# Performance work log

Hardware: AMD Instinct MI355X
Metric: run time of the kernel (lower is better)

## Reference

```python
import jax, jax.numpy as jnp
import numpy as np
import math

D_MODEL = 1024
FEAT = 16            # feature_dim
HEADS = 16
HEAD_DIM = D_MODEL // HEADS          # 64
EXP = 1 + FEAT + FEAT * FEAT         # 273, expanded (Taylor) feature dim
BATCH = 4
SEQ = 2048


def taylor_exp(x):
    """2nd-order Taylor feature map: [1, x/d^{1/4}, (x ox x)/(sqrt(2)*sqrt(d))]."""
    d = x.shape[-1]
    r2 = math.sqrt(2.0)
    rd = math.sqrt(d)
    rrd = math.sqrt(rd)
    x2 = (x[..., :, None] * x[..., None, :]).reshape(*x.shape[:-1], d * d) / r2
    return jnp.concatenate([jnp.ones_like(x[..., :1]), x / rrd, x2 / rd], axis=-1)


def setup_inputs() -> dict:
    key = jax.random.key(0)
    ks = jax.random.split(key, 9)
    s_in = 1.0 / math.sqrt(D_MODEL)
    inp = {
        "x": jax.random.normal(ks[0], (BATCH, SEQ, D_MODEL), dtype=jnp.float32),
        "kv_state": jnp.zeros((BATCH, HEADS, EXP, HEAD_DIM), dtype=jnp.float32),
        "k_state": jnp.zeros((BATCH, HEADS, EXP), dtype=jnp.float32),
        # Linear params stored as [in, out] (y = x @ W + b)
        "Wq": jax.random.normal(ks[1], (D_MODEL, FEAT * HEADS), dtype=jnp.float32) * s_in,
        "bq": jnp.zeros((FEAT * HEADS,), dtype=jnp.float32),
        "Wk": jax.random.normal(ks[2], (D_MODEL, FEAT * HEADS), dtype=jnp.float32) * s_in,
        "bk": jnp.zeros((FEAT * HEADS,), dtype=jnp.float32),
        "Wv": jax.random.normal(ks[3], (D_MODEL, HEAD_DIM * HEADS), dtype=jnp.float32) * s_in,
        "bv": jnp.zeros((HEAD_DIM * HEADS,), dtype=jnp.float32),
        "Wo": jax.random.normal(ks[4], (HEADS * HEAD_DIM, D_MODEL), dtype=jnp.float32) * s_in,
        "bo": jnp.zeros((D_MODEL,), dtype=jnp.float32),
    }
    return inp


def _forward(x, kv_state, k_state, Wq, bq, Wk, bk, Wv, bv, Wo, bo):
    b, l, _ = x.shape
    # projections -> b h l d
    q = (x @ Wq + bq).reshape(b, l, HEADS, FEAT).transpose(0, 2, 1, 3)
    k = (x @ Wk + bk).reshape(b, l, HEADS, FEAT).transpose(0, 2, 1, 3)
    v = (x @ Wv + bv).reshape(b, l, HEADS, HEAD_DIM).transpose(0, 2, 1, 3)
    q = taylor_exp(q)  # b h l EXP
    k = taylor_exp(k)  # b h l EXP

    # scan over time: carry (kv_state [b,h,EXP,hd], k_state [b,h,EXP])
    qs = jnp.moveaxis(q, 2, 0)  # l b h EXP
    ks = jnp.moveaxis(k, 2, 0)  # l b h EXP
    vs = jnp.moveaxis(v, 2, 0)  # l b h hd

    def step(carry, qkv_t):
        kv, kst = carry
        q_t, k_t, v_t = qkv_t
        kv = kv + k_t[..., :, None] * v_t[..., None, :]   # b h EXP hd
        kst = kst + k_t                                    # b h EXP
        num = jnp.einsum('bhd,bhdc->bhc', q_t, kv)
        den = jnp.einsum('bhd,bhd->bh', q_t, kst) + 1e-6
        return (kv, kst), num / den[..., None]

    (kv_f, kst_f), outs = jax.lax.scan(step, (kv_state, k_state), (qs, ks, vs))
    # outs: l b h hd -> b l (h hd)
    y = jnp.moveaxis(outs, 0, 1).reshape(b, l, HEADS * HEAD_DIM)
    y = y @ Wo + bo  # dropout is identity in eval mode
    return y, kv_f, kst_f


def reference(x, kv_state, k_state, Wq, bq, Wk, bk, Wv, bv, Wo, bo):
    return _forward(x, kv_state, k_state, Wq, bq, Wk, bk, Wv, bv, Wo, bo)
```

## Files before the change

### kernel.cpp

```cpp
#include <hip/hip_runtime.h>

typedef unsigned short u16;
typedef __attribute__((ext_vector_type(8))) short bf16x8;
typedef __attribute__((ext_vector_type(4))) float f32x4;

#define BATCH 4
#define SEQ   2048
#define DM    1024
#define HEADS 16
#define FEAT  16
#define HD    64
#define EXPD  273
#define EXPP  288
#define CHK   128
#define NC    16
#define BH    64
#define QKS   512
#define MROWS 8192
#define C2    0.17677669529663687f

__device__ __forceinline__ u16 f2b(float f) {
  union { float f; unsigned u; } v; v.f = f;
  unsigned u = v.u;
  return (u16)((u + 0x7fffu + ((u >> 16) & 1u)) >> 16);
}
__device__ __forceinline__ float b2f(u16 s) {
  union { unsigned u; float f; } v; v.u = ((unsigned)s) << 16; return v.f;
}

typedef const unsigned int __attribute__((address_space(1)))* gas1;
typedef unsigned int __attribute__((address_space(3)))* las3;
__device__ __forceinline__ void gl_lds16(const u16* g, u16* l) {
  __builtin_amdgcn_global_load_lds((gas1)(const void*)g, (las3)(void*)l, 16, 0, 0);
}

__global__ __launch_bounds__(256) void prep(const float* __restrict__ x, u16* __restrict__ xb,
                                            const float* __restrict__ Wq, const float* __restrict__ Wk,
                                            const float* __restrict__ Wv, const float* __restrict__ Wo,
                                            u16* __restrict__ wqkT, u16* __restrict__ wvT, u16* __restrict__ woT,
                                            const float* __restrict__ bq, const float* __restrict__ bk,
                                            float* __restrict__ bqk) {
  __shared__ float tile[32][33];
  int id = blockIdx.x;
  if (id < 8192) {
    int i = id * 256 + threadIdx.x;
    float4 v = ((const float4*)x)[i];
    u16 r[4] = {f2b(v.x), f2b(v.y), f2b(v.z), f2b(v.w)};
    ((uint2*)xb)[i] = *(uint2*)r;
    return;
  }
  id -= 8192;
  if (id < 2560) {
    const float* src; u16* dst; int N, t;
    if (id < 256)       { src = Wq; dst = wqkT;            N = 256;  t = id; }
    else if (id < 512)  { src = Wk; dst = wqkT + 256 * DM; N = 256;  t = id - 256; }
    else if (id < 1536) { src = Wv; dst = wvT;             N = 1024; t = id - 512; }
    else                { src = Wo; dst = woT;             N = 1024; t = id - 1536; }
    int nt = N / 32;
    int n0 = (t % nt) * 32, k0 = (t / nt) * 32;
    int tx = threadIdx.x & 31, ty = threadIdx.x >> 5;
    for (int i = ty; i < 32; i += 8)
      tile[i][tx] = src[(size_t)(k0 + i) * N + n0 + tx];
    __syncthreads();
    for (int i = ty; i < 32; i += 8)
      dst[(size_t)(n0 + i) * DM + k0 + tx] = f2b(tile[tx][i]);
    return;
  }
  int i = threadIdx.x;
  bqk[i] = bq[i];
  bqk[256 + i] = bk[i];
}

__global__ __launch_bounds__(256) void gemm128(const u16* __restrict__ A, const u16* __restrict__ BT,
                                               const float* __restrict__ bias, int M, int N, int K,
                                               float* __restrict__ outF, u16* __restrict__ outB,
                                               u16* __restrict__ outT) {
  __shared__ __align__(16) u16 As[128 * 32];
  __shared__ __align__(16) u16 Bs[128 * 32];
  const int tid = threadIdx.x;
  const int wave = tid >> 6, lane = tid & 63, qd = lane >> 4, ln = lane & 15;
  const int wr = (wave >> 1) * 64, wc = (wave & 1) * 64;
  const int m0 = blockIdx.y * 128, n0 = blockIdx.x * 128;
  f32x4 acc[4][4];
#pragma unroll
  for (int i = 0; i < 4; i++)
#pragma unroll
    for (int j = 0; j < 4; j++) acc[i][j] = (f32x4){0.f, 0.f, 0.f, 0.f};
  const int sr = tid >> 2, sk = (tid & 3) * 8;
  const u16* gA0 = A + (size_t)(m0 + sr) * K + sk;
  const u16* gA1 = A + (size_t)(m0 + 64 + sr) * K + sk;
  const u16* gB0 = BT + (size_t)(n0 + sr) * K + sk;
  const u16* gB1 = BT + (size_t)(n0 + 64 + sr) * K + sk;
  u16* lA0 = &As[(size_t)(wave * 64) * 8];
  u16* lA1 = &As[(size_t)(256 + wave * 64) * 8];
  u16* lB0 = &Bs[(size_t)(wave * 64) * 8];
  u16* lB1 = &Bs[(size_t)(256 + wave * 64) * 8];
  for (int kk = 0; kk < K; kk += 32) {
    gl_lds16(gA0 + kk, lA0);
    gl_lds16(gA1 + kk, lA1);
    gl_lds16(gB0 + kk, lB0);
    gl_lds16(gB1 + kk, lB1);
    __syncthreads();
    bf16x8 af[4], bf[4];
#pragma unroll
    for (int t = 0; t < 4; t++) {
      af[t] = *(const bf16x8*)&As[(wr + t * 16 + ln) * 32 + qd * 8];
      bf[t] = *(const bf16x8*)&Bs[(wc + t * 16 + ln) * 32 + qd * 8];
    }
#pragma unroll
    for (int mt = 0; mt < 4; mt++)
#pragma unroll
      for (int nt = 0; nt < 4; nt++)
        acc[mt][nt] = __builtin_amdgcn_mfma_f32_16x16x32_bf16(af[mt], bf[nt], acc[mt][nt], 0, 0, 0);
    __syncthreads();
  }
  if (outT) {
#pragma unroll
    for (int nt = 0; nt < 4; nt++) {
      int col = n0 + wc + nt * 16 + ln;
      float bv = bias[col];
#pragma unroll
      for (int mt = 0; mt < 4; mt++) {
        u16 pk[4];
#pragma unroll
        for (int r = 0; r < 4; r++) pk[r] = f2b(acc[mt][nt][r] + bv);
        int row0 = m0 + wr + mt * 16 + qd * 4;
        *(uint2*)&outT[(size_t)col * M + row0] = *(uint2*)pk;
      }
    }
    return;
  }
#pragma unroll
  for (int nt = 0; nt < 4; nt++) {
    int col = n0 + wc + nt * 16 + ln;
    float bv = bias[col];
#pragma unroll
    for (int mt = 0; mt < 4; mt++) {
#pragma unroll
      for (int r = 0; r < 4; r++) {
        int row = m0 + wr + mt * 16 + qd * 4 + r;
        float v = acc[mt][nt][r] + bv;
        if (outF) outF[(size_t)row * N + col] = v;
        else      outB[(size_t)row * N + col] = f2b(v);
      }
    }
  }
}

template<int KT>
__device__ __forceinline__ void feat_row(const float* q16, int p, u16* dst) {
  u16 pk[16];
  if (KT == 0 && p == 0) {
    pk[0] = 0x3F80;
#pragma unroll
    for (int j = 1; j < 16; j++) pk[j] = f2b(0.5f * q16[j - 1]);
  } else if (KT == 0) {
    pk[0] = f2b(0.5f * q16[15]);
    float wm = C2 * q16[0];
#pragma unroll
    for (int j = 1; j < 16; j++) pk[j] = f2b(wm * q16[j - 1]);
  } else {
    constexpr int c = 2 * KT;
    float wm = C2 * (p ? q16[c]     : q16[c - 1]);
    float w0 = C2 * (p ? q16[c - 1] : q16[c - 2]);
    pk[0] = f2b(w0 * q16[15]);
#pragma unroll
    for (int j = 1; j < 16; j++) pk[j] = f2b(wm * q16[j - 1]);
    if (KT == 8 && p) {
#pragma unroll
      for (int j = 1; j < 16; j++) pk[j] = 0;
    }
  }
  *(uint4*)dst = *(uint4*)pk;
  *(uint4*)(dst + 8) = *(uint4*)(pk + 8);
}

template<int MTB>
__device__ __forceinline__ void kfeat(const float* k16, int p, int t2, u16 (*kfT)[16][136]) {
  u16 pk[16];
  if (MTB == 0 && true) {
    if (p == 0) {
      pk[0] = 0x3F80;
#pragma unroll
      for (int j = 1; j < 16; j++) pk[j] = f2b(0.5f * k16[j - 1]);
    } else {
      float w0 = C2 * k16[0], wm = C2 * k16[1];
      pk[0] = f2b(w0 * k16[15]);
#pragma unroll
      for (int j = 1; j < 16; j++) pk[j] = f2b(wm * k16[j - 1]);
    }
  } else if (MTB == 1) {
    if (p == 0) {
      pk[0] = f2b(0.5f * k16[15]);
      float wm = C2 * k16[0];
#pragma unroll
      for (int j = 1; j < 16; j++) pk[j] = f2b(wm * k16[j - 1]);
    } else {
      float w0 = C2 * k16[1], wm = C2 * k16[2];
      pk[0] = f2b(w0 * k16[15]);
#pragma unroll
      for (int j = 1; j < 16; j++) pk[j] = f2b(wm * k16[j - 1]);
    }
  } else {
    float wm = C2 * (p ? k16[MTB + 1] : k16[MTB - 1]);
    float w0 = C2 * (p ? k16[MTB]     : k16[MTB - 2]);
    pk[0] = f2b(w0 * k16[15]);
#pragma unroll
    for (int j = 1; j < 16; j++) pk[j] = f2b(wm * k16[j - 1]);
  }
  int b = 2 * p + (MTB & 1);
#pragma unroll
  for (int el = 0; el < 16; el++) kfT[b][el][t2] = pk[el];
}

__global__ __launch_bounds__(256) void chunk_sums(const float* __restrict__ qkw, const u16* __restrict__ vbT,
                                                  u16* __restrict__ ckvT, float* __restrict__ ck) {
  __shared__ float kl[CHK][20];
  __shared__ __align__(16) u16 kfT[4][16][136];
  const int tid = threadIdx.x;
  const int bh = blockIdx.x / NC, c = blockIdx.x % NC;
  const int b = bh >> 4, h = bh & 15;
  const int wave = tid >> 6, lane = tid & 63, qd = lane >> 4, ln = lane & 15;
  const int t2 = tid >> 1, p = tid & 1;
  const size_t rowbase = (size_t)(b * SEQ + c * CHK);
  float k16[16];
  {
    const float* kp = &qkw[(rowbase + t2) * QKS + 256 + h * FEAT];
    float4 v0 = *(const float4*)kp, v1 = *(const float4*)(kp + 4);
    float4 v2 = *(const float4*)(kp + 8), v3 = *(const float4*)(kp + 12);
    k16[0] = v0.x; k16[1] = v0.y; k16[2] = v0.z; k16[3] = v0.w;
    k16[4] = v1.x; k16[5] = v1.y; k16[6] = v1.z; k16[7] = v1.w;
    k16[8] = v2.x; k16[9] = v2.y; k16[10] = v2.z; k16[11] = v2.w;
    k16[12] = v3.x; k16[13] = v3.y; k16[14] = v3.z; k16[15] = v3.w;
    float4 h0, h1;
    if (p == 0) { h0 = v0; h1 = v1; } else { h0 = v2; h1 = v3; }
    *(float4*)&kl[t2][p * 8] = h0;
    *(float4*)&kl[t2][p * 8 + 4] = h1;
  }
  uint4 bVv[4][4];
#pragma unroll
  for (int kk2 = 0; kk2 < 4; kk2++)
#pragma unroll
    for (int nt = 0; nt < 4; nt++)
      bVv[kk2][nt] = *(const uint4*)&vbT[(size_t)(h * HD + nt * 16 + ln) * MROWS +
                                         rowbase + kk2 * 32 + qd * 8];
  const size_t obase = (size_t)(bh * NC + c) * HD;
  auto mstore = [&](int mt, int bufw) {
    f32x4 acc[4];
#pragma unroll
    for (int nt = 0; nt < 4; nt++) acc[nt] = (f32x4){0.f, 0.f, 0.f, 0.f};
#pragma unroll
    for (int kk2 = 0; kk2 < 4; kk2++) {
      bf16x8 a = *(const bf16x8*)&kfT[bufw][ln][kk2 * 32 + qd * 8];
#pragma unroll
      for (int nt = 0; nt < 4; nt++) {
        bf16x8 bb = *(const bf16x8*)&bVv[kk2][nt];
        acc[nt] = __builtin_amdgcn_mfma_f32_16x16x32_bf16(a, bb, acc[nt], 0, 0, 0);
      }
    }
#pragma unroll
    for (int nt = 0; nt < 4; nt++) {
      u16 pk[4];
#pragma unroll
      for (int r = 0; r < 4; r++) pk[r] = f2b(acc[nt][r]);
      *(uint2*)&ckvT[(obase + nt * 16 + ln) * EXPP + mt * 16 + qd * 4] = *(uint2*)pk;
    }
  };
  __syncthreads();
  kfeat<0>(k16, p, t2, kfT); kfeat<1>(k16, p, t2, kfT);
  __syncthreads();
  mstore(wave, wave);
  __syncthreads();
  kfeat<4>(k16, p, t2, kfT); kfeat<5>(k16, p, t2, kfT);
  __syncthreads();
  mstore(4 + wave, wave);
  __syncthreads();
  kfeat<8>(k16, p, t2, kfT); kfeat<9>(k16, p, t2, kfT);
  __syncthreads();
  mstore(8 + wave, wave);
  __syncthreads();
  kfeat<12>(k16, p, t2, kfT); kfeat<13>(k16, p, t2, kfT);
  __syncthreads();
  mstore(12 + wave, wave);
  __syncthreads();
  {
    u16 pk[16];
    if (p == 0) {
      float w0 = C2 * k16[14], wm = C2 * k16[15];
      pk[0] = f2b(w0 * k16[15]);
#pragma unroll
      for (int j = 1; j < 16; j++) pk[j] = f2b(wm * k16[j - 1]);
    } else {
      pk[0] = f2b(C2 * k16[15] * k16[15]);
#pragma unroll
      for (int j = 1; j < 16; j++) pk[j] = 0;
    }
#pragma unroll
    for (int el = 0; el < 16; el++) kfT[p][el][t2] = pk[el];
  }
  __syncthreads();
  if (wave < 2) mstore(16 + wave, wave);
  for (int e = tid; e < EXPP; e += 256) {
    float s = 0.f;
    if (e == 0) s = (float)CHK;
    else if (e < 17) { float t = 0.f; for (int tt = 0; tt < CHK; tt++) t += kl[tt][e - 1]; s = 0.5f * t; }
    else if (e < EXPD) {
      int u = e - 17, i0 = u >> 4, j0 = u & 15; float t = 0.f;
      for (int tt = 0; tt < CHK; tt++) t += kl[tt][i0] * kl[tt][j0];
      s = C2 * t;
    }
    ck[(size_t)(bh * NC + c) * EXPP + e] = s;
  }
}

__global__ __launch_bounds__(256) void kv_prefix(u16* __restrict__ ckvT, const float* __restrict__ kv0,
                                                 float* __restrict__ out_kv,
                                                 float* __restrict__ ck, const float* __restrict__ k0,
                                                 float* __restrict__ out_k) {
  const int tid = threadIdx.x;
  const int bh = blockIdx.x / 10, eg = blockIdx.x % 10;
  if (eg == 9) {
    for (int e = tid; e < EXPP; e += 256) {
      float S = (e < EXPD) ? k0[(size_t)bh * EXPD + e] : 0.f;
      for (int c = 0; c < NC; c++) {
        size_t idx = ((size_t)bh * NC + c) * EXPP + e;
        float v = ck[idx];
        ck[idx] = S;
        S += v;
      }
      if (e < EXPD) out_k[(size_t)bh * EXPD + e] = S;
    }
    return;
  }
  const int hd = tid >> 2;
  const int e0 = eg * 32 + (tid & 3) * 8;
  float S[8];
#pragma unroll
  for (int j = 0; j < 8; j++) {
    int e = e0 + j;
    S[j] = (e < EXPD) ? kv0[((size_t)bh * EXPD + e) * HD + hd] : 0.f;
  }
  u16* base = ckvT + ((size_t)bh * NC * HD + hd) * EXPP + e0;
  const size_t cstride = (size_t)HD * EXPP;
  uint4 v0 = *(const uint4*)base;
  uint4 v1 = *(const uint4*)(base + cstride);
  for (int c = 0; c < NC; c++) {
    uint4 vn = v1;
    if (c + 2 < NC) vn = *(const uint4*)(base + (size_t)(c + 2) * cstride);
    union { uint4 q; u16 s[8]; } pk;
#pragma unroll
    for (int j = 0; j < 8; j++) pk.s[j] = f2b(S[j]);
    *(uint4*)(base + (size_t)c * cstride) = pk.q;
    union { uint4 q; u16 s[8]; } vv; vv.q = v0;
#pragma unroll
    for (int j = 0; j < 8; j++) S[j] += b2f(vv.s[j]);
    v0 = v1; v1 = vn;
  }
#pragma unroll
  for (int j = 0; j < 8; j++) {
    int e = e0 + j;
    if (e < EXPD) out_kv[((size_t)bh * EXPD + e) * HD + hd] = S[j];
  }
}

__global__ __launch_bounds__(256) void out_chunk(const float* __restrict__ qkw, const u16* __restrict__ vbT,
                                                 const u16* __restrict__ ckvT, const float* __restrict__ ck,
                                                 u16* __restrict__ ob) {
  __shared__ __align__(16) u16 pool[4 * CHK * 40];
  __shared__ float kstl[EXPP];
  __shared__ float denl[CHK];
  u16 (*qlb)[40] = (u16(*)[40])pool;
  u16 (*klb)[40] = (u16(*)[40])(pool + CHK * 40);
  u16 (*qfs)[CHK][40] = (u16(*)[CHK][40])(pool + 2 * CHK * 40);
  u16 (*al)[136] = (u16(*)[136])pool;
  const int tid = threadIdx.x;
  const int bh = blockIdx.x / NC, c = blockIdx.x % NC;
  const int b = bh >> 4, h = bh & 15;
  const int wave = tid >> 6, lane = tid & 63, qd = lane >> 4, ln = lane & 15;
  const int t2 = tid >> 1, p = tid & 1;
  const size_t rowbase = (size_t)(b * SEQ + c * CHK);
  float q16[16];
  {
    const float* qp = &qkw[(rowbase + t2) * QKS + h * FEAT];
    float4 v0 = *(const float4*)qp, v1 = *(const float4*)(qp + 4);
    float4 v2 = *(const float4*)(qp + 8), v3 = *(const float4*)(qp + 12);
    q16[0] = v0.x; q16[1] = v0.y; q16[2] = v0.z; q16[3] = v0.w;
    q16[4] = v1.x; q16[5] = v1.y; q16[6] = v1.z; q16[7] = v1.w;
    q16[8] = v2.x; q16[9] = v2.y; q16[10] = v2.z; q16[11] = v2.w;
    q16[12] = v3.x; q16[13] = v3.y; q16[14] = v3.z; q16[15] = v3.w;
    u16 qb[8];
#pragma unroll
    for (int j = 0; j < 8; j++) qb[j] = f2b(q16[p * 8 + j]);
    *(uint4*)&qlb[t2][p * 8] = *(uint4*)qb;
    *(uint4*)&qlb[t2][16 + p * 8] = (uint4){0u, 0u, 0u, 0u};
    const float* kp = &qkw[(rowbase + t2) * QKS + 256 + h * FEAT + p * 8];
    float4 k0v = *(const float4*)kp, k1v = *(const float4*)(kp + 4);
    u16 kb[8] = {f2b(k0v.x), f2b(k0v.y), f2b(k0v.z), f2b(k0v.w),
                 f2b(k1v.x), f2b(k1v.y), f2b(k1v.z), f2b(k1v.w)};
    *(uint4*)&klb[t2][p * 8] = *(uint4*)kb;
    *(uint4*)&klb[t2][16 + p * 8] = (uint4){0u, 0u, 0u, 0u};
  }
  const size_t cbase = (size_t)(bh * NC + c);
  for (int e = tid; e < EXPP; e += 256) kstl[e] = ck[cbase * EXPP + e];
  const u16* sptr = ckvT + (cbase * HD + wave * 16 + ln) * EXPP + qd * 8;
  uint4 bSv[9];
#pragma unroll
  for (int kt = 0; kt < 9; kt++) bSv[kt] = *(const uint4*)(sptr + kt * 32);
  uint4 bVv[4];
#pragma unroll
  for (int kk2 = 0; kk2 < 4; kk2++)
    bVv[kk2] = *(const uint4*)&vbT[(size_t)(h * HD + wave * 16 + ln) * MROWS +
                                   rowbase + kk2 * 32 + qd * 8];
  feat_row<0>(q16, p, &qfs[0][t2][p * 16]);
  __syncthreads();
  f32x4 accO[8];
#pragma unroll
  for (int mt = 0; mt < 8; mt++) accO[mt] = (f32x4){0.f, 0.f, 0.f, 0.f};
#define KSTEP(KT)                                                                          \
  {                                                                                        \
    if ((KT) < 8) feat_row<(KT) + 1>(q16, p, &qfs[((KT) + 1) & 1][t2][p * 16]);            \
    bf16x8 bS = *(const bf16x8*)&bSv[(KT)];                                                \
    _Pragma("unroll")                                                                      \
    for (int mt = 0; mt < 8; mt++) {                                                       \
      bf16x8 a = *(const bf16x8*)&qfs[(KT) & 1][mt * 16 + ln][qd * 8];                     \
      accO[mt] = __builtin_amdgcn_mfma_f32_16x16x32_bf16(a, bS, accO[mt], 0, 0, 0);        \
    }                                                                                      \
    __syncthreads();                                                                       \
  }
  KSTEP(0) KSTEP(1) KSTEP(2) KSTEP(3) KSTEP(4) KSTEP(5) KSTEP(6) KSTEP(7) KSTEP(8)
#undef KSTEP
  f32x4 accU[8][2];
#pragma unroll
  for (int st2 = 0; st2 < 2; st2++) {
    bf16x8 bU = *(const bf16x8*)&klb[(wave + st2 * 4) * 16 + ln][qd * 8];
#pragma unroll
    for (int mt = 0; mt < 8; mt++) {
      bf16x8 aU = *(const bf16x8*)&qlb[mt * 16 + ln][qd * 8];
      accU[mt][st2] = __builtin_amdgcn_mfma_f32_16x16x32_bf16(aU, bU, (f32x4){0.f, 0.f, 0.f, 0.f}, 0, 0, 0);
    }
  }
  __syncthreads();
#pragma unroll
  for (int mt = 0; mt < 8; mt++)
#pragma unroll
    for (int st2 = 0; st2 < 2; st2++)
#pragma unroll
      for (int r = 0; r < 4; r++) {
        int t = mt * 16 + qd * 4 + r, s = (wave + st2 * 4) * 16 + ln;
        float u = accU[mt][st2][r];
        float sc = 1.f + 0.25f * u + 0.03125f * u * u;
        al[t][s] = f2b((s <= t) ? sc : 0.f);
      }
  __syncthreads();
#pragma unroll
  for (int kk2 = 0; kk2 < 4; kk2++) {
    bf16x8 bb = *(const bf16x8*)&bVv[kk2];
#pragma unroll
    for (int mt = 0; mt < 8; mt++) {
      bf16x8 a = *(const bf16x8*)&al[mt * 16 + ln][kk2 * 32 + qd * 8];
      accO[mt] = __builtin_amdgcn_mfma_f32_16x16x32_bf16(a, bb, accO[mt], 0, 0, 0);
    }
  }
  {
    float s = 0.f;
#pragma unroll
    for (int i2 = 0; i2 < 8; i2++) {
      int i = p * 8 + i2;
      float inner = 0.f;
#pragma unroll
      for (int j = 0; j < 16; j++) inner += q16[j] * kstl[17 + i * 16 + j];
      s += q16[i] * inner;
    }
    s *= C2;
    float s1 = 0.f;
#pragma unroll
    for (int j2 = 0; j2 < 8; j2++) s1 += q16[p * 8 + j2] * kstl[1 + p * 8 + j2];
    s += 0.5f * s1;
    if (p == 0) s += kstl[0] + 1e-6f;
    float da = 0.f;
#pragma unroll
    for (int sb = 0; sb < 8; sb++) {
      union { uint4 q; u16 hh[8]; } uu;
      uu.q = *(const uint4*)&al[t2][p * 64 + sb * 8];
#pragma unroll
      for (int j = 0; j < 8; j++) da += b2f(uu.hh[j]);
    }
    s += da;
    s += __shfl_xor(s, 1);
    if (p == 0) denl[t2] = s;
  }
  __syncthreads();
#pragma unroll
  for (int mt = 0; mt < 8; mt++)
#pragma unroll
    for (int r = 0; r < 4; r++) {
      int t = mt * 16 + qd * 4 + r;
      ob[(rowbase + t) * DM + h * HD + wave * 16 + ln] = f2b(accO[mt][r] / denl[t]);
    }
}

extern "C" void kernel_launch(void* const* d_in, const int* in_sizes, int n_in,
                              void* d_out, int out_size, void* d_ws, size_t ws_size,
                              hipStream_t stream) {
  (void)in_sizes; (void)n_in; (void)out_size;
  const float* x   = (const float*)d_in[0];
  const float* kv0 = (const float*)d_in[1];
  const float* k0  = (const float*)d_in[2];
  const float* bq  = (const float*)d_in[4];
  const float* bk  = (const float*)d_in[6];
  const float* bv  = (const float*)d_in[8];
  const float* bo  = (const float*)d_in[10];
  float* out = (float*)d_out;
  char* ws = (char*)d_ws;
  size_t off = 0;
  auto take = [&](size_t bytes) { char* p = ws + off; off += (bytes + 255) & ~(size_t)255; return p; };
  u16*   xb   = (u16*)  take((size_t)BATCH * SEQ * DM * 2);
  u16*   wqkT = (u16*)  take((size_t)QKS * DM * 2);
  u16*   wvT  = (u16*)  take((size_t)DM * DM * 2);
  u16*   woT  = (u16*)  take((size_t)DM * DM * 2);
  float* bqk  = (float*)take((size_t)QKS * 4);
  float* qkw  = (float*)take((size_t)BATCH * SEQ * QKS * 4);
  u16*   vbT  = (u16*)  take((size_t)BATCH * SEQ * DM * 2);
  u16*   ckvT = (u16*)  take((size_t)BH * NC * EXPP * HD * 2);
  float* ck   = (float*)take((size_t)BH * NC * EXPP * 4);
  u16*   ob   = (u16*)  take((size_t)BATCH * SEQ * DM * 2);
  if (off > ws_size) return;

  float* out_kv = out + (size_t)BATCH * SEQ * DM;
  float* out_k  = out_kv + (size_t)BH * EXPD * HD;

  prep<<<8192 + 2560 + 1, 256, 0, stream>>>(x, xb,
      (const float*)d_in[3], (const float*)d_in[5], (const float*)d_in[7], (const float*)d_in[9],
      wqkT, wvT, woT, bq, bk, bqk);

  gemm128<<<dim3(4, 64), 256, 0, stream>>>(xb, wqkT, bqk, MROWS, QKS, DM, qkw, nullptr, nullptr);
  gemm128<<<dim3(8, 64), 256, 0, stream>>>(xb, wvT,  bv,  MROWS, DM,  DM, nullptr, nullptr, vbT);

  chunk_sums<<<BH * NC, 256, 0, stream>>>(qkw, vbT, ckvT, ck);
  kv_prefix<<<BH * 10, 256, 0, stream>>>(ckvT, kv0, out_kv, ck, k0, out_k);
  out_chunk<<<BH * NC, 256, 0, stream>>>(qkw, vbT, ckvT, ck, ob);

  gemm128<<<dim3(8, 64), 256, 0, stream>>>(ob, woT, bo, MROWS, DM, DM, out, nullptr, nullptr);
}
```

Measured before the change: 305.7 us.

## Fuse Q/K/V projections into one GEMM and restructure out_chunk MFMA layout

```diff
diff --git a/kernel.cpp b/kernel.cpp
--- a/kernel.cpp
+++ b/kernel.cpp
@@ -37,9 +37,9 @@
 __global__ __launch_bounds__(256) void prep(const float* __restrict__ x, u16* __restrict__ xb,
                                             const float* __restrict__ Wq, const float* __restrict__ Wk,
                                             const float* __restrict__ Wv, const float* __restrict__ Wo,
-                                            u16* __restrict__ wqkT, u16* __restrict__ wvT, u16* __restrict__ woT,
+                                            u16* __restrict__ wqkvT, u16* __restrict__ woT,
                                             const float* __restrict__ bq, const float* __restrict__ bk,
-                                            float* __restrict__ bqk) {
+                                            const float* __restrict__ bv, float* __restrict__ bias_all) {
   __shared__ float tile[32][33];
   int id = blockIdx.x;
   if (id < 8192) {
@@ -52,10 +52,10 @@
   id -= 8192;
   if (id < 2560) {
     const float* src; u16* dst; int N, t;
-    if (id < 256)       { src = Wq; dst = wqkT;            N = 256;  t = id; }
-    else if (id < 512)  { src = Wk; dst = wqkT + 256 * DM; N = 256;  t = id - 256; }
-    else if (id < 1536) { src = Wv; dst = wvT;             N = 1024; t = id - 512; }
-    else                { src = Wo; dst = woT;             N = 1024; t = id - 1536; }
+    if (id < 256)       { src = Wq; dst = wqkvT;            N = 256;  t = id; }
+    else if (id < 512)  { src = Wk; dst = wqkvT + 256 * DM; N = 256;  t = id - 256; }
+    else if (id < 1536) { src = Wv; dst = wqkvT + 512 * DM; N = 1024; t = id - 512; }
+    else                { src = Wo; dst = woT;              N = 1024; t = id - 1536; }
     int nt = N / 32;
     int n0 = (t % nt) * 32, k0 = (t / nt) * 32;
     int tx = threadIdx.x & 31, ty = threadIdx.x >> 5;
@@ -66,21 +66,25 @@
       dst[(size_t)(n0 + i) * DM + k0 + tx] = f2b(tile[tx][i]);
     return;
   }
-  int i = threadIdx.x;
-  bqk[i] = bq[i];
-  bqk[256 + i] = bk[i];
-}
-
-__global__ __launch_bounds__(256) void gemm128(const u16* __restrict__ A, const u16* __restrict__ BT,
-                                               const float* __restrict__ bias, int M, int N, int K,
-                                               float* __restrict__ outF, u16* __restrict__ outB,
-                                               u16* __restrict__ outT) {
+  id -= 2560;
+  int i = id * 256 + threadIdx.x;
+  float v;
+  if (i < 256) v = bq[i];
+  else if (i < 512) v = bk[i - 256];
+  else v = bv[i - 512];
+  bias_all[i] = v;
+}
+
+__global__ __launch_bounds__(256) void gemmQKV(const u16* __restrict__ A, const u16* __restrict__ BT,
+                                               const float* __restrict__ bias,
+                                               float* __restrict__ qkw, u16* __restrict__ vbT) {
   __shared__ __align__(16) u16 As[128 * 32];
   __shared__ __align__(16) u16 Bs[128 * 32];
   const int tid = threadIdx.x;
   const int wave = tid >> 6, lane = tid & 63, qd = lane >> 4, ln = lane & 15;
   const int wr = (wave >> 1) * 64, wc = (wave & 1) * 64;
   const int m0 = blockIdx.y * 128, n0 = blockIdx.x * 128;
+  const int K = DM;
   f32x4 acc[4][4];
 #pragma unroll
   for (int i = 0; i < 4; i++)
@@ -114,36 +118,90 @@
         acc[mt][nt] = __builtin_amdgcn_mfma_f32_16x16x32_bf16(af[mt], bf[nt], acc[mt][nt], 0, 0, 0);
     __syncthreads();
   }
-  if (outT) {
+  if (n0 < 512) {
 #pragma unroll
     for (int nt = 0; nt < 4; nt++) {
       int col = n0 + wc + nt * 16 + ln;
       float bv = bias[col];
 #pragma unroll
+      for (int mt = 0; mt < 4; mt++)
+#pragma unroll
+        for (int r = 0; r < 4; r++) {
+          int row = m0 + wr + mt * 16 + qd * 4 + r;
+          qkw[(size_t)row * QKS + col] = acc[mt][nt][r] + bv;
+        }
+    }
+  } else {
+#pragma unroll
+    for (int nt = 0; nt < 4; nt++) {
+      int col = n0 + wc + nt * 16 + ln;
+      float bv = bias[col];
+      int vcol = col - 512;
+#pragma unroll
       for (int mt = 0; mt < 4; mt++) {
         u16 pk[4];
 #pragma unroll
         for (int r = 0; r < 4; r++) pk[r] = f2b(acc[mt][nt][r] + bv);
         int row0 = m0 + wr + mt * 16 + qd * 4;
-        *(uint2*)&outT[(size_t)col * M + row0] = *(uint2*)pk;
+        *(uint2*)&vbT[(size_t)vcol * MROWS + row0] = *(uint2*)pk;
       }
     }
-    return;
+  }
+}
+
+__global__ __launch_bounds__(256) void gemm128(const u16* __restrict__ A, const u16* __restrict__ BT,
+                                               const float* __restrict__ bias, int M, int N, int K,
+                                               float* __restrict__ outF) {
+  __shared__ __align__(16) u16 As[128 * 32];
+  __shared__ __align__(16) u16 Bs[128 * 32];
+  const int tid = threadIdx.x;
+  const int wave = tid >> 6, lane = tid & 63, qd = lane >> 4, ln = lane & 15;
+  const int wr = (wave >> 1) * 64, wc = (wave & 1) * 64;
+  const int m0 = blockIdx.y * 128, n0 = blockIdx.x * 128;
+  f32x4 acc[4][4];
+#pragma unroll
+  for (int i = 0; i < 4; i++)
+#pragma unroll
+    for (int j = 0; j < 4; j++) acc[i][j] = (f32x4){0.f, 0.f, 0.f, 0.f};
+  const int sr = tid >> 2, sk = (tid & 3) * 8;
+  const u16* gA0 = A + (size_t)(m0 + sr) * K + sk;
+  const u16* gA1 = A + (size_t)(m0 + 64 + sr) * K + sk;
+  const u16* gB0 = BT + (size_t)(n0 + sr) * K + sk;
+  const u16* gB1 = BT + (size_t)(n0 + 64 + sr) * K + sk;
+  u16* lA0 = &As[(size_t)(wave * 64) * 8];
+  u16* lA1 = &As[(size_t)(256 + wave * 64) * 8];
+  u16* lB0 = &Bs[(size_t)(wave * 64) * 8];
+  u16* lB1 = &Bs[(size_t)(256 + wave * 64) * 8];
+  for (int kk = 0; kk < K; kk += 32) {
+    gl_lds16(gA0 + kk, lA0);
+    gl_lds16(gA1 + kk, lA1);
+    gl_lds16(gB0 + kk, lB0);
+    gl_lds16(gB1 + kk, lB1);
+    __syncthreads();
+    bf16x8 af[4], bf[4];
+#pragma unroll
+    for (int t = 0; t < 4; t++) {
+      af[t] = *(const bf16x8*)&As[(wr + t * 16 + ln) * 32 + qd * 8];
+      bf[t] = *(const bf16x8*)&Bs[(wc + t * 16 + ln) * 32 + qd * 8];
+    }
+#pragma unroll
+    for (int mt = 0; mt < 4; mt++)
+#pragma unroll
+      for (int nt = 0; nt < 4; nt++)
+        acc[mt][nt] = __builtin_amdgcn_mfma_f32_16x16x32_bf16(af[mt], bf[nt], acc[mt][nt], 0, 0, 0);
+    __syncthreads();
   }
 #pragma unroll
   for (int nt = 0; nt < 4; nt++) {
     int col = n0 + wc + nt * 16 + ln;
     float bv = bias[col];
 #pragma unroll
-    for (int mt = 0; mt < 4; mt++) {
+    for (int mt = 0; mt < 4; mt++)
 #pragma unroll
       for (int r = 0; r < 4; r++) {
         int row = m0 + wr + mt * 16 + qd * 4 + r;
-        float v = acc[mt][nt][r] + bv;
-        if (outF) outF[(size_t)row * N + col] = v;
-        else      outB[(size_t)row * N + col] = f2b(v);
+        outF[(size_t)row * N + col] = acc[mt][nt][r] + bv;
       }
-    }
   }
 }
 
@@ -178,7 +236,7 @@
 template<int MTB>
 __device__ __forceinline__ void kfeat(const float* k16, int p, int t2, u16 (*kfT)[16][136]) {
   u16 pk[16];
-  if (MTB == 0 && true) {
+  if (MTB == 0) {
     if (p == 0) {
       pk[0] = 0x3F80;
 #pragma unroll
@@ -366,13 +424,14 @@
 __global__ __launch_bounds__(256) void out_chunk(const float* __restrict__ qkw, const u16* __restrict__ vbT,
                                                  const u16* __restrict__ ckvT, const float* __restrict__ ck,
                                                  u16* __restrict__ ob) {
-  __shared__ __align__(16) u16 pool[4 * CHK * 40];
+  __shared__ __align__(16) u16 pool[18432];
   __shared__ float kstl[EXPP];
   __shared__ float denl[CHK];
   u16 (*qlb)[40] = (u16(*)[40])pool;
-  u16 (*klb)[40] = (u16(*)[40])(pool + CHK * 40);
-  u16 (*qfs)[CHK][40] = (u16(*)[CHK][40])(pool + 2 * CHK * 40);
-  u16 (*al)[136] = (u16(*)[136])pool;
+  u16 (*klb)[32] = (u16(*)[32])(pool + 5120);
+  u16 (*qfs)[40] = (u16(*)[40])(pool + 9216);
+  u16 (*alB)[72] = (u16(*)[72])pool;
+  u16 (*alA)[72] = (u16(*)[72])(pool + 9216);
   const int tid = threadIdx.x;
   const int bh = blockIdx.x / NC, c = blockIdx.x % NC;
   const int b = bh >> 4, h = bh & 15;
@@ -411,54 +470,79 @@
   for (int kk2 = 0; kk2 < 4; kk2++)
     bVv[kk2] = *(const uint4*)&vbT[(size_t)(h * HD + wave * 16 + ln) * MROWS +
                                    rowbase + kk2 * 32 + qd * 8];
-  feat_row<0>(q16, p, &qfs[0][t2][p * 16]);
+  feat_row<0>(q16, p, &qfs[t2][p * 16]);
   __syncthreads();
   f32x4 accO[8];
 #pragma unroll
-  for (int mt = 0; mt < 8; mt++) accO[mt] = (f32x4){0.f, 0.f, 0.f, 0.f};
+  for (int nt = 0; nt < 8; nt++) accO[nt] = (f32x4){0.f, 0.f, 0.f, 0.f};
 #define KSTEP(KT)                                                                          \
   {                                                                                        \
-    if ((KT) < 8) feat_row<(KT) + 1>(q16, p, &qfs[((KT) + 1) & 1][t2][p * 16]);            \
-    bf16x8 bS = *(const bf16x8*)&bSv[(KT)];                                                \
+    bf16x8 aS = *(const bf16x8*)&bSv[(KT)];                                                \
     _Pragma("unroll")                                                                      \
-    for (int mt = 0; mt < 8; mt++) {                                                       \
-      bf16x8 a = *(const bf16x8*)&qfs[(KT) & 1][mt * 16 + ln][qd * 8];                     \
-      accO[mt] = __builtin_amdgcn_mfma_f32_16x16x32_bf16(a, bS, accO[mt], 0, 0, 0);        \
+    for (int nt = 0; nt < 8; nt++) {                                                       \
+      bf16x8 bQ = *(const bf16x8*)&qfs[nt * 16 + ln][qd * 8];                              \
+      accO[nt] = __builtin_amdgcn_mfma_f32_16x16x32_bf16(aS, bQ, accO[nt], 0, 0, 0);       \
     }                                                                                      \
     __syncthreads();                                                                       \
+    if ((KT) < 8) {                                                                        \
+      feat_row<(KT) + 1>(q16, p, &qfs[t2][p * 16]);                                        \
+      __syncthreads();                                                                     \
+    }                                                                                      \
   }
   KSTEP(0) KSTEP(1) KSTEP(2) KSTEP(3) KSTEP(4) KSTEP(5) KSTEP(6) KSTEP(7) KSTEP(8)
 #undef KSTEP
-  f32x4 accU[8][2];
-#pragma unroll
-  for (int st2 = 0; st2 < 2; st2++) {
-    bf16x8 bU = *(const bf16x8*)&klb[(wave + st2 * 4) * 16 + ln][qd * 8];
-#pragma unroll
-    for (int mt = 0; mt < 8; mt++) {
-      bf16x8 aU = *(const bf16x8*)&qlb[mt * 16 + ln][qd * 8];
-      accU[mt][st2] = __builtin_amdgcn_mfma_f32_16x16x32_bf16(aU, bU, (f32x4){0.f, 0.f, 0.f, 0.f}, 0, 0, 0);
-    }
-  }
-  __syncthreads();
-#pragma unroll
-  for (int mt = 0; mt < 8; mt++)
-#pragma unroll
-    for (int st2 = 0; st2 < 2; st2++)
+  {
+    f32x4 accU[8];
+    bf16x8 aK = *(const bf16x8*)&klb[wave * 16 + ln][qd * 8];
+#pragma unroll
+    for (int nt = 0; nt < 8; nt++) {
+      bf16x8 bQ = *(const bf16x8*)&qlb[nt * 16 + ln][qd * 8];
+      accU[nt] = __builtin_amdgcn_mfma_f32_16x16x32_bf16(aK, bQ, (f32x4){0.f, 0.f, 0.f, 0.f}, 0, 0, 0);
+    }
+#pragma unroll
+    for (int nt = 0; nt < 8; nt++) {
+      int t = nt * 16 + ln, sb = wave * 16 + qd * 4;
+      u16 pk[4];
 #pragma unroll
       for (int r = 0; r < 4; r++) {
-        int t = mt * 16 + qd * 4 + r, s = (wave + st2 * 4) * 16 + ln;
-        float u = accU[mt][st2][r];
+        float u = accU[nt][r];
         float sc = 1.f + 0.25f * u + 0.03125f * u * u;
-        al[t][s] = f2b((s <= t) ? sc : 0.f);
+        pk[r] = (sb + r <= t) ? f2b(sc) : (u16)0;
       }
+      *(uint2*)&alA[t][sb] = *(uint2*)pk;
+    }
+  }
+  {
+    f32x4 accU[8];
+    bf16x8 aK = *(const bf16x8*)&klb[(wave + 4) * 16 + ln][qd * 8];
+#pragma unroll
+    for (int nt = 0; nt < 8; nt++) {
+      bf16x8 bQ = *(const bf16x8*)&qlb[nt * 16 + ln][qd * 8];
+      accU[nt] = __builtin_amdgcn_mfma_f32_16x16x32_bf16(aK, bQ, (f32x4){0.f, 0.f, 0.f, 0.f}, 0, 0, 0);
+    }
+    __syncthreads();
+#pragma unroll
+    for (int nt = 0; nt < 8; nt++) {
+      int t = nt * 16 + ln, sbl = wave * 16 + qd * 4;
+      u16 pk[4];
+#pragma unroll
+      for (int r = 0; r < 4; r++) {
+        float u = accU[nt][r];
+        float sc = 1.f + 0.25f * u + 0.03125f * u * u;
+        pk[r] = (64 + sbl + r <= t) ? f2b(sc) : (u16)0;
+      }
+      *(uint2*)&alB[t][sbl] = *(uint2*)pk;
+    }
+  }
   __syncthreads();
 #pragma unroll
   for (int kk2 = 0; kk2 < 4; kk2++) {
-    bf16x8 bb = *(const bf16x8*)&bVv[kk2];
-#pragma unroll
-    for (int mt = 0; mt < 8; mt++) {
-      bf16x8 a = *(const bf16x8*)&al[mt * 16 + ln][kk2 * 32 + qd * 8];
-      accO[mt] = __builtin_amdgcn_mfma_f32_16x16x32_bf16(a, bb, accO[mt], 0, 0, 0);
+    bf16x8 aV = *(const bf16x8*)&bVv[kk2];
+#pragma unroll
+    for (int nt = 0; nt < 8; nt++) {
+      bf16x8 bA = (kk2 < 2) ? *(const bf16x8*)&alA[nt * 16 + ln][kk2 * 32 + qd * 8]
+                            : *(const bf16x8*)&alB[nt * 16 + ln][(kk2 - 2) * 32 + qd * 8];
+      accO[nt] = __builtin_amdgcn_mfma_f32_16x16x32_bf16(aV, bA, accO[nt], 0, 0, 0);
     }
   }
   {
@@ -477,11 +561,12 @@
     for (int j2 = 0; j2 < 8; j2++) s1 += q16[p * 8 + j2] * kstl[1 + p * 8 + j2];
     s += 0.5f * s1;
     if (p == 0) s += kstl[0] + 1e-6f;
+    const u16* arow = p ? &alB[t2][0] : &alA[t2][0];
     float da = 0.f;
 #pragma unroll
     for (int sb = 0; sb < 8; sb++) {
       union { uint4 q; u16 hh[8]; } uu;
-      uu.q = *(const uint4*)&al[t2][p * 64 + sb * 8];
+      uu.q = *(const uint4*)(arow + sb * 8);
 #pragma unroll
       for (int j = 0; j < 8; j++) da += b2f(uu.hh[j]);
     }
@@ -491,12 +576,14 @@
   }
   __syncthreads();
 #pragma unroll
-  for (int mt = 0; mt < 8; mt++)
-#pragma unroll
-    for (int r = 0; r < 4; r++) {
-      int t = mt * 16 + qd * 4 + r;
-      ob[(rowbase + t) * DM + h * HD + wave * 16 + ln] = f2b(accO[mt][r] / denl[t]);
-    }
+  for (int nt = 0; nt < 8; nt++) {
+    int t = nt * 16 + ln;
+    float dn = denl[t];
+    u16 pk[4];
+#pragma unroll
+    for (int r = 0; r < 4; r++) pk[r] = f2b(accO[nt][r] / dn);
+    *(uint2*)&ob[(rowbase + t) * DM + h * HD + wave * 16 + qd * 4] = *(uint2*)pk;
+  }
 }
 
 extern "C" void kernel_launch(void* const* d_in, const int* in_sizes, int n_in,
@@ -514,31 +601,29 @@
   char* ws = (char*)d_ws;
   size_t off = 0;
   auto take = [&](size_t bytes) { char* p = ws + off; off += (bytes + 255) & ~(size_t)255; return p; };
-  u16*   xb   = (u16*)  take((size_t)BATCH * SEQ * DM * 2);
-  u16*   wqkT = (u16*)  take((size_t)QKS * DM * 2);
-  u16*   wvT  = (u16*)  take((size_t)DM * DM * 2);
-  u16*   woT  = (u16*)  take((size_t)DM * DM * 2);
-  float* bqk  = (float*)take((size_t)QKS * 4);
-  float* qkw  = (float*)take((size_t)BATCH * SEQ * QKS * 4);
-  u16*   vbT  = (u16*)  take((size_t)BATCH * SEQ * DM * 2);
-  u16*   ckvT = (u16*)  take((size_t)BH * NC * EXPP * HD * 2);
-  float* ck   = (float*)take((size_t)BH * NC * EXPP * 4);
-  u16*   ob   = (u16*)  take((size_t)BATCH * SEQ * DM * 2);
+  u16*   xb     = (u16*)  take((size_t)BATCH * SEQ * DM * 2);
+  u16*   wqkvT  = (u16*)  take((size_t)1536 * DM * 2);
+  u16*   woT    = (u16*)  take((size_t)DM * DM * 2);
+  float* bias_a = (float*)take((size_t)1536 * 4);
+  float* qkw    = (float*)take((size_t)BATCH * SEQ * QKS * 4);
+  u16*   vbT    = (u16*)  take((size_t)BATCH * SEQ * DM * 2);
+  u16*   ckvT   = (u16*)  take((size_t)BH * NC * EXPP * HD * 2);
+  float* ck     = (float*)take((size_t)BH * NC * EXPP * 4);
+  u16*   ob     = (u16*)  take((size_t)BATCH * SEQ * DM * 2);
   if (off > ws_size) return;
 
   float* out_kv = out + (size_t)BATCH * SEQ * DM;
   float* out_k  = out_kv + (size_t)BH * EXPD * HD;
 
-  prep<<<8192 + 2560 + 1, 256, 0, stream>>>(x, xb,
+  prep<<<8192 + 2560 + 6, 256, 0, stream>>>(x, xb,
       (const float*)d_in[3], (const float*)d_in[5], (const float*)d_in[7], (const float*)d_in[9],
-      wqkT, wvT, woT, bq, bk, bqk);
-
-  gemm128<<<dim3(4, 64), 256, 0, stream>>>(xb, wqkT, bqk, MROWS, QKS, DM, qkw, nullptr, nullptr);
-  gemm128<<<dim3(8, 64), 256, 0, stream>>>(xb, wvT,  bv,  MROWS, DM,  DM, nullptr, nullptr, vbT);
+      wqkvT, woT, bq, bk, bv, bias_a);
+
+  gemmQKV<<<dim3(12, 64), 256, 0, stream>>>(xb, wqkvT, bias_a, qkw, vbT);
 
   chunk_sums<<<BH * NC, 256, 0, stream>>>(qkw, vbT, ckvT, ck);
   kv_prefix<<<BH * 10, 256, 0, stream>>>(ckvT, kv0, out_kv, ck, k0, out_k);
   out_chunk<<<BH * NC, 256, 0, stream>>>(qkw, vbT, ckvT, ck, ob);
 
-  gemm128<<<dim3(8, 64), 256, 0, stream>>>(ob, woT, bo, MROWS, DM, DM, out, nullptr, nullptr);
-}
+  gemm128<<<dim3(8, 64), 256, 0, stream>>>(ob, woT, bo, MROWS, DM, DM, out);
+}
```

Result: faster. 291.2 us (-4.7%).
